# Performance work log

Hardware: AMD Instinct MI355X
Metric: run time of the kernel (lower is better)

## Reference

```python
import jax, jax.numpy as jnp
import numpy as np

M, K, N = 1024, 8192, 8192
PACK = 16  # 16 two-bit codes per int32 word


def _pack_ternary(codes):
    # codes: (N, K) int32 with values in {0,1,3} -> (N, K//16) int32
    c = codes.reshape(N, K // PACK, PACK).astype(jnp.uint32)
    shifts = (jnp.arange(PACK, dtype=jnp.uint32) * 2)
    packed = jnp.sum(c << shifts, axis=-1, dtype=jnp.uint32)
    return jax.lax.bitcast_convert_type(packed, jnp.int32)


def setup_inputs() -> dict:
    key = jax.random.key(0)
    kx, kw, kb = jax.random.split(key, 3)
    x = jax.random.normal(kx, (M, K), dtype=jnp.float16)
    # ternary codes drawn from {0,1,3} (code 2 is unused by the format)
    vals = jnp.array([0, 1, 3], dtype=jnp.int32)
    codes = vals[jax.random.randint(kw, (N, K), 0, 3)]
    packed_w = _pack_ternary(codes)
    bias = jax.random.normal(kb, (N,), dtype=jnp.float16)
    return {"x": x, "packed_w": packed_w, "bias": bias}


def _unpack(packed_w):
    # (N, K//16) int32 -> (N, K) fp16 weights with values in {0,1,3}
    shifts = jnp.arange(PACK, dtype=jnp.int32) * 2
    w = (packed_w[:, :, None] >> shifts) & 3  # mask keeps low 2 bits even with arithmetic shift
    return w.reshape(packed_w.shape[0], -1).astype(jnp.float16)


def reference(x, packed_w, bias):
    w = _unpack(packed_w)  # (N, K)
    # Y = X W^T + b, fp32 accumulation as in the CUDA/Triton GEMM, fp16 output
    y = jnp.einsum('mk,nk->mn', x, w, preferred_element_type=jnp.float32)
    y = y.astype(jnp.float16) + bias
    return y
```

## Files before the change

### kernel.cpp

```cpp
#include <hip/hip_runtime.h>
#include <hip/hip_fp16.h>
#include <stdint.h>

#define M_DIM 1024
#define N_DIM 8192
#define K_DIM 8192
#define KP    (K_DIM / 16)

#define BM 128
#define BN 128
#define BK 64
#define NTHREADS 256
#define B_STRIDE 144

#define MT_STRIDE 2097152
#define KT_STRIDE 16384

typedef _Float16 half8   __attribute__((ext_vector_type(8)));
typedef __fp16   fp16x2  __attribute__((ext_vector_type(2)));
typedef float    f32x4   __attribute__((ext_vector_type(4)));
typedef float    f32x16  __attribute__((ext_vector_type(16)));

__device__ __forceinline__ uint32_t cvt2(float a, float b) {
  fp16x2 p = __builtin_amdgcn_cvt_pkrtz(a, b);
  return __builtin_bit_cast(uint32_t, p);
}

__device__ __forceinline__ void gload_lds16(const char* g, char* l) {
  __builtin_amdgcn_global_load_lds(
      (const __attribute__((address_space(1))) void*)g,
      (__attribute__((address_space(3))) void*)l, 16, 0, 0);
}

__device__ __forceinline__ half8 dec_frag(uint32_t word, uint32_t sh) {
  const uint32_t T = 0x42063C00u;
  uint32_t h  = (word >> sh) & 0xFFFFu;
  uint32_t W  = (h & 0x3333u) | ((h << 14) & 0x33330000u);
  uint32_t c0 = __builtin_amdgcn_perm(0u, W, 0x04040200u);
  uint32_t c1 = __builtin_amdgcn_perm(0u, W, 0x04040301u);
  uint32_t s0 = (c0 * 0x1001u) & 0x03030303u;
  uint32_t s1 = (c1 * 0x1001u) & 0x03030303u;
  uint32_t P0 = __builtin_amdgcn_perm(0u, T, s0);
  uint32_t P1 = __builtin_amdgcn_perm(0u, T, s1);
  uint4 v;
  v.x = __builtin_amdgcn_perm(P0, 0u, 0x05000400u);
  v.y = __builtin_amdgcn_perm(P0, 0u, 0x07000600u);
  v.z = __builtin_amdgcn_perm(P1, 0u, 0x05000400u);
  v.w = __builtin_amdgcn_perm(P1, 0u, 0x07000600u);
  return __builtin_bit_cast(half8, v);
}

__global__ __launch_bounds__(256)
void cvt_x_t(const float* __restrict__ x, char* __restrict__ xhT) {
  __shared__ __align__(16) char st[16384];
  const int b  = blockIdx.x;
  const int mt = b >> 7, kt = b & 127;
  const int t  = threadIdx.x;
#pragma unroll
  for (int p = 0; p < 8; ++p) {
    int f   = t + 256 * p;
    int R   = f >> 4;
    int cc4 = f & 15;
    float4 v = *(const float4*)(x + (size_t)(mt * 128 + R) * K_DIM + kt * 64 + cc4 * 4);
    uint32_t w0 = cvt2(v.x, v.y), w1 = cvt2(v.z, v.w);
    int c8 = cc4 >> 1, hh = cc4 & 1;
    int i32 = R >> 5, r = R & 31, ks = c8 >> 1, q = c8 & 1;
    *(uint2*)(st + i32 * 4096 + ks * 1024 + q * 512 + r * 16 + hh * 8) = make_uint2(w0, w1);
  }
  __syncthreads();
  char* outb = xhT + (size_t)mt * MT_STRIDE + (size_t)kt * KT_STRIDE;
#pragma unroll
  for (int e = 0; e < 4; ++e) {
    int d = (e * 256 + t) * 16;
    *(uint4*)(outb + d) = *(const uint4*)(st + d);
  }
}

__global__ __launch_bounds__(NTHREADS, 2)
void ternary_gemm_dc(const char* __restrict__ xhT,
                     const int*  __restrict__ pw,
                     const float* __restrict__ bias,
                     float*       __restrict__ out) {
  __shared__ __align__(16) char Ast[3 * 16384];
  __shared__ __align__(16) char stg[3 * 2048];

  const int tid  = threadIdx.x;
  const int lane = tid & 63;
  const int w    = tid >> 6;
  const int wm   = w >> 1, wn = w & 1;
  const int bid  = blockIdx.x;
  const int mt   = bid & 7;
  const int bm   = mt * BM;
  const int bn   = (bid >> 3) * BN;

  const char* gAs = xhT + (size_t)mt * MT_STRIDE + w * 4096 + lane * 16;

  const int rT = tid >> 1, hT = tid & 1;
  const int2* gB = (const int2*)pw + (size_t)(bn + rT) * (KP / 2) + hT;
  const int stOff = rT * 16 + hT * 8;

  int rowOff[2];
#pragma unroll
  for (int j = 0; j < 2; ++j)
    rowOff[j] = (wn * 64 + j * 32 + (lane & 31)) * 16;
  const uint32_t sh = (lane >> 5) * 16;

  const char* const aPtr = Ast + wm * 8192 + lane * 16;

  f32x16 acc[2][2];
#pragma unroll
  for (int i = 0; i < 2; ++i)
#pragma unroll
    for (int j = 0; j < 2; ++j) acc[i][j] = (f32x16)(0.f);

  const int NT = K_DIM / BK;

  auto stageA = [&](int buf, int kt) {
    const char* g = gAs + (size_t)kt * KT_STRIDE;
    char* lbase = Ast + buf * 16384 + w * 4096;
#pragma unroll
    for (int e = 0; e < 4; ++e)
      gload_lds16(g + e * 1024, lbase + e * 1024);
  };

  stageA(0, 0);
  stageA(1, 1);
  int2 w0 = gB[0];
  *(int2*)(stg + stOff) = w0;
  int2 wcur = gB[2];
  __syncthreads();

  int2 wnxt;
  auto step = [&](int cur, int kt, bool counted) {
    if (kt + 2 < NT) stageA((cur + 2) % 3, kt + 2);

    uint32_t wr0[4], wr1[4];
    *(uint4*)wr0 = *(const uint4*)(stg + cur * 2048 + rowOff[0]);
    *(uint4*)wr1 = *(const uint4*)(stg + cur * 2048 + rowOff[1]);
    *(int2*)(stg + ((cur + 1) % 3) * 2048 + stOff) = wcur;
    int kn2 = (kt + 2 < NT) ? (kt + 2) : (NT - 1);
    wnxt = gB[kn2 * 2];

#pragma unroll
    for (int ks = 0; ks < 4; ++ks) {
      half8 a0 = *(const half8*)(aPtr + cur * 16384 + 0 * 4096 + ks * 1024);
      half8 a1 = *(const half8*)(aPtr + cur * 16384 + 1 * 4096 + ks * 1024);
      half8 bf0 = dec_frag(wr0[ks], sh);
      half8 bf1 = dec_frag(wr1[ks], sh);
      acc[0][0] = __builtin_amdgcn_mfma_f32_32x32x16_f16(a0, bf0, acc[0][0], 0, 0, 0);
      acc[0][1] = __builtin_amdgcn_mfma_f32_32x32x16_f16(a0, bf1, acc[0][1], 0, 0, 0);
      acc[1][0] = __builtin_amdgcn_mfma_f32_32x32x16_f16(a1, bf0, acc[1][0], 0, 0, 0);
      acc[1][1] = __builtin_amdgcn_mfma_f32_32x32x16_f16(a1, bf1, acc[1][1], 0, 0, 0);
    }

    if (counted) {
      __builtin_amdgcn_sched_barrier(0);
      asm volatile("s_waitcnt vmcnt(5) lgkmcnt(0)" ::: "memory");
      __builtin_amdgcn_s_barrier();
      asm volatile("" ::: "memory");
      __builtin_amdgcn_sched_barrier(0);
    } else {
      __syncthreads();
    }
    wcur = wnxt;
  };

  for (int kt = 0; kt < NT - 2; kt += 3) {
    step(0, kt, true);
    step(1, kt + 1, true);
    step(2, kt + 2, true);
  }
  step(0, NT - 2, false);
  step(1, NT - 1, false);

#pragma unroll
  for (int j = 0; j < 2; ++j) {
    int n = bn + wn * 64 + j * 32 + (lane & 31);
    __half hb = __float2half_rn(bias[n]);
#pragma unroll
    for (int i = 0; i < 2; ++i) {
      int mbase = bm + wm * 64 + i * 32 + 4 * (lane >> 5);
#pragma unroll
      for (int reg = 0; reg < 16; ++reg) {
        int m = mbase + (reg & 3) + 8 * (reg >> 2);
        __half hy = __float2half_rn(acc[i][j][reg]);
        out[(size_t)m * N_DIM + n] = __half2float(__hadd(hy, hb));
      }
    }
  }
}

__device__ __forceinline__ uint32_t unpack_pair16(uint32_t u, int p) {
  uint32_t c0 = (u >> (4 * p)) & 3u;
  uint32_t c1 = (u >> (4 * p + 2)) & 3u;
  uint32_t lo = (c0 & 1u) * 0x3C00u + (c0 >> 1) * 0x0600u;
  uint32_t hi = (c1 & 1u) * 0x3C00u + (c1 >> 1) * 0x0600u;
  return lo | (hi << 16);
}

__global__ __launch_bounds__(NTHREADS, 2)
void ternary_gemm(const float* __restrict__ x,
                  const int*   __restrict__ pw,
                  const float* __restrict__ bias,
                  float*       __restrict__ out) {
  __shared__ __align__(16) char AsB[128 * B_STRIDE];
  __shared__ __align__(16) char BsB[128 * B_STRIDE];

  const int tid  = threadIdx.x;
  const int lane = tid & 63;
  const int w    = tid >> 6;
  const int wm   = w >> 1, wn = w & 1;
  const int bid  = blockIdx.x;
  const int bm   = (bid & 7) * 128;
  const int bn   = (bid >> 3) * 128;

  const int rT = tid >> 1, hT = tid & 1;
  const float* gA = x + (size_t)(bm + rT) * K_DIM + hT * 32;
  char* const  lA = AsB + rT * B_STRIDE + hT * 64;
  const int2* gB = (const int2*)pw + (size_t)(bn + rT) * (KP / 2) + hT;
  char* dBp[4];
#pragma unroll
  for (int h = 0; h < 4; ++h)
    dBp[h] = BsB + rT * B_STRIDE + (hT * 4 + h) * 16;

  int offA[4][2], offB[4][2];
#pragma unroll
  for (int i = 0; i < 4; ++i)
#pragma unroll
    for (int ks = 0; ks < 2; ++ks) {
      int c = ks * 4 + (lane >> 4);
      offA[i][ks] = (wm * 64 + i * 16 + (lane & 15)) * B_STRIDE + c * 16;
      offB[i][ks] = (wn * 64 + i * 16 + (lane & 15)) * B_STRIDE + c * 16;
    }

  f32x4 acc[4][4];
#pragma unroll
  for (int i = 0; i < 4; ++i)
#pragma unroll
    for (int j = 0; j < 4; ++j)
      acc[i][j] = (f32x4){0.f, 0.f, 0.f, 0.f};

  const int NT = K_DIM / BK;
  for (int kt = 0; kt < NT; ++kt) {
    __syncthreads();
    int2 wcur = gB[kt * 2];
    float4 av[8];
#pragma unroll
    for (int v = 0; v < 8; ++v) av[v] = *(const float4*)(gA + kt * BK + v * 4);
    uint32_t d0[8], d1[8];
#pragma unroll
    for (int p = 0; p < 8; ++p) d0[p] = unpack_pair16((uint32_t)wcur.x, p);
#pragma unroll
    for (int p = 0; p < 8; ++p) d1[p] = unpack_pair16((uint32_t)wcur.y, p);
    *(uint4*)dBp[0] = make_uint4(d0[0], d0[1], d0[2], d0[3]);
    *(uint4*)dBp[1] = make_uint4(d0[4], d0[5], d0[6], d0[7]);
    *(uint4*)dBp[2] = make_uint4(d1[0], d1[1], d1[2], d1[3]);
    *(uint4*)dBp[3] = make_uint4(d1[4], d1[5], d1[6], d1[7]);
#pragma unroll
    for (int v = 0; v < 4; ++v) {
      uint4 aw;
      aw.x = cvt2(av[2 * v].x, av[2 * v].y);
      aw.y = cvt2(av[2 * v].z, av[2 * v].w);
      aw.z = cvt2(av[2 * v + 1].x, av[2 * v + 1].y);
      aw.w = cvt2(av[2 * v + 1].z, av[2 * v + 1].w);
      *(uint4*)(lA + v * 16) = aw;
    }
    __syncthreads();
#pragma unroll
    for (int ks = 0; ks < 2; ++ks) {
      half8 af[4], bf[4];
#pragma unroll
      for (int i = 0; i < 4; ++i) af[i] = *(const half8*)(AsB + offA[i][ks]);
#pragma unroll
      for (int j = 0; j < 4; ++j) bf[j] = *(const half8*)(BsB + offB[j][ks]);
#pragma unroll
      for (int i = 0; i < 4; ++i)
#pragma unroll
        for (int j = 0; j < 4; ++j)
          acc[i][j] = __builtin_amdgcn_mfma_f32_16x16x32_f16(af[i], bf[j], acc[i][j], 0, 0, 0);
    }
  }
#pragma unroll
  for (int j = 0; j < 4; ++j) {
    int n = bn + wn * 64 + j * 16 + (lane & 15);
    __half hb = __float2half_rn(bias[n]);
#pragma unroll
    for (int i = 0; i < 4; ++i) {
      int m0 = bm + wm * 64 + i * 16 + (lane >> 4) * 4;
#pragma unroll
      for (int r = 0; r < 4; ++r) {
        __half hy = __float2half_rn(acc[i][j][r]);
        out[(size_t)(m0 + r) * N_DIM + n] = __half2float(__hadd(hy, hb));
      }
    }
  }
}

extern "C" void kernel_launch(void* const* d_in, const int* in_sizes, int n_in,
                              void* d_out, int out_size, void* d_ws, size_t ws_size,
                              hipStream_t stream) {
  (void)in_sizes; (void)n_in; (void)out_size;
  const float* x    = (const float*)d_in[0];
  const int*   pwp  = (const int*)d_in[1];
  const float* bias = (const float*)d_in[2];
  float*       outp = (float*)d_out;

  const size_t need = (size_t)M_DIM * K_DIM * 2;
  if (ws_size >= need) {
    char* xhT = (char*)d_ws;
    cvt_x_t<<<8 * 128, 256, 0, stream>>>(x, xhT);
    dim3 grid((M_DIM / BM) * (N_DIM / BN));
    ternary_gemm_dc<<<grid, NTHREADS, 0, stream>>>(xhT, pwp, bias, outp);
  } else {
    dim3 grid((M_DIM / 128) * (N_DIM / 128));
    ternary_gemm<<<grid, NTHREADS, 0, stream>>>(x, pwp, bias, outp);
  }
}
```

Before: 234.5 us.

## Load packed ternary weights straight into registers, drop LDS staging

```diff
diff --git a/kernel.cpp b/kernel.cpp
--- a/kernel.cpp
+++ b/kernel.cpp
@@ -82,7 +82,6 @@
                      const float* __restrict__ bias,
                      float*       __restrict__ out) {
   __shared__ __align__(16) char Ast[3 * 16384];
-  __shared__ __align__(16) char stg[3 * 2048];
 
   const int tid  = threadIdx.x;
   const int lane = tid & 63;
@@ -95,14 +94,8 @@
 
   const char* gAs = xhT + (size_t)mt * MT_STRIDE + w * 4096 + lane * 16;
 
-  const int rT = tid >> 1, hT = tid & 1;
-  const int2* gB = (const int2*)pw + (size_t)(bn + rT) * (KP / 2) + hT;
-  const int stOff = rT * 16 + hT * 8;
-
-  int rowOff[2];
-#pragma unroll
-  for (int j = 0; j < 2; ++j)
-    rowOff[j] = (wn * 64 + j * 32 + (lane & 31)) * 16;
+  const uint4* pB0 = (const uint4*)pw + (size_t)(bn + wn * 64 + (lane & 31)) * (KP / 4);
+  const uint4* pB1 = pB0 + 32 * (KP / 4);
   const uint32_t sh = (lane >> 5) * 16;
 
   const char* const aPtr = Ast + wm * 8192 + lane * 16;
@@ -125,53 +118,64 @@
 
   stageA(0, 0);
   stageA(1, 1);
-  int2 w0 = gB[0];
-  *(int2*)(stg + stOff) = w0;
-  int2 wcur = gB[2];
+  uint4 cA0 = pB0[0], cA1 = pB1[0];
+  uint4 cB0, cB1;
   __syncthreads();
 
-  int2 wnxt;
-  auto step = [&](int cur, int kt, bool counted) {
-    if (kt + 2 < NT) stageA((cur + 2) % 3, kt + 2);
-
-    uint32_t wr0[4], wr1[4];
-    *(uint4*)wr0 = *(const uint4*)(stg + cur * 2048 + rowOff[0]);
-    *(uint4*)wr1 = *(const uint4*)(stg + cur * 2048 + rowOff[1]);
-    *(int2*)(stg + ((cur + 1) % 3) * 2048 + stOff) = wcur;
-    int kn2 = (kt + 2 < NT) ? (kt + 2) : (NT - 1);
-    wnxt = gB[kn2 * 2];
-
+  auto step = [&](int cur, int kt, uint4& c0, uint4& c1, uint4& n0, uint4& n1,
+                  bool counted) {
+    int knb = (kt + 1 < NT) ? kt + 1 : NT - 1;
+    n0 = pB0[knb];
+    n1 = pB1[knb];
+    if (kt + 2 < NT) stageA((kt + 2) % 3, kt + 2);
+
+    half8 a0[4], a1[4];
 #pragma unroll
     for (int ks = 0; ks < 4; ++ks) {
-      half8 a0 = *(const half8*)(aPtr + cur * 16384 + 0 * 4096 + ks * 1024);
-      half8 a1 = *(const half8*)(aPtr + cur * 16384 + 1 * 4096 + ks * 1024);
-      half8 bf0 = dec_frag(wr0[ks], sh);
-      half8 bf1 = dec_frag(wr1[ks], sh);
-      acc[0][0] = __builtin_amdgcn_mfma_f32_32x32x16_f16(a0, bf0, acc[0][0], 0, 0, 0);
-      acc[0][1] = __builtin_amdgcn_mfma_f32_32x32x16_f16(a0, bf1, acc[0][1], 0, 0, 0);
-      acc[1][0] = __builtin_amdgcn_mfma_f32_32x32x16_f16(a1, bf0, acc[1][0], 0, 0, 0);
-      acc[1][1] = __builtin_amdgcn_mfma_f32_32x32x16_f16(a1, bf1, acc[1][1], 0, 0, 0);
-    }
+      a0[ks] = *(const half8*)(aPtr + cur * 16384 + 0 * 4096 + ks * 1024);
+      a1[ks] = *(const half8*)(aPtr + cur * 16384 + 1 * 4096 + ks * 1024);
+    }
+
+    uint32_t wd0[4] = {c0.x, c0.y, c0.z, c0.w};
+    uint32_t wd1[4] = {c1.x, c1.y, c1.z, c1.w};
+    half8 bf0[4], bf1[4];
+#pragma unroll
+    for (int ks = 0; ks < 4; ++ks) {
+      bf0[ks] = dec_frag(wd0[ks], sh);
+      bf1[ks] = dec_frag(wd1[ks], sh);
+    }
+
+    __builtin_amdgcn_s_setprio(1);
+#pragma unroll
+    for (int ks = 0; ks < 4; ++ks) {
+      acc[0][0] = __builtin_amdgcn_mfma_f32_32x32x16_f16(a0[ks], bf0[ks], acc[0][0], 0, 0, 0);
+      acc[0][1] = __builtin_amdgcn_mfma_f32_32x32x16_f16(a0[ks], bf1[ks], acc[0][1], 0, 0, 0);
+      acc[1][0] = __builtin_amdgcn_mfma_f32_32x32x16_f16(a1[ks], bf0[ks], acc[1][0], 0, 0, 0);
+      acc[1][1] = __builtin_amdgcn_mfma_f32_32x32x16_f16(a1[ks], bf1[ks], acc[1][1], 0, 0, 0);
+    }
+    __builtin_amdgcn_s_setprio(0);
 
     if (counted) {
       __builtin_amdgcn_sched_barrier(0);
-      asm volatile("s_waitcnt vmcnt(5) lgkmcnt(0)" ::: "memory");
+      asm volatile("s_waitcnt vmcnt(6) lgkmcnt(0)" ::: "memory");
       __builtin_amdgcn_s_barrier();
       asm volatile("" ::: "memory");
       __builtin_amdgcn_sched_barrier(0);
     } else {
       __syncthreads();
     }
-    wcur = wnxt;
   };
 
-  for (int kt = 0; kt < NT - 2; kt += 3) {
-    step(0, kt, true);
-    step(1, kt + 1, true);
-    step(2, kt + 2, true);
-  }
-  step(0, NT - 2, false);
-  step(1, NT - 1, false);
+  for (int kt = 0; kt < NT - 2; kt += 6) {
+    step(0, kt,     cA0, cA1, cB0, cB1, true);
+    step(1, kt + 1, cB0, cB1, cA0, cA1, true);
+    step(2, kt + 2, cA0, cA1, cB0, cB1, true);
+    step(0, kt + 3, cB0, cB1, cA0, cA1, true);
+    step(1, kt + 4, cA0, cA1, cB0, cB1, true);
+    step(2, kt + 5, cB0, cB1, cA0, cA1, true);
+  }
+  step(0, NT - 2, cA0, cA1, cB0, cB1, false);
+  step(1, NT - 1, cB0, cB1, cA0, cA1, false);
 
 #pragma unroll
   for (int j = 0; j < 2; ++j) {
```

After: 245.2 us. 1.05x slower.

## Shrink GEMM tile to 64x128 with per-wave 64x32 outputs and higher occupancy

Applied to the files above, without the earlier changes.

```diff
diff --git a/kernel.cpp b/kernel.cpp
--- a/kernel.cpp
+++ b/kernel.cpp
@@ -7,7 +7,7 @@
 #define K_DIM 8192
 #define KP    (K_DIM / 16)
 
-#define BM 128
+#define BM 64
 #define BN 128
 #define BK 64
 #define NTHREADS 256
@@ -76,86 +76,80 @@
   }
 }
 
-__global__ __launch_bounds__(NTHREADS, 2)
+__global__ __launch_bounds__(NTHREADS, 4)
 void ternary_gemm_dc(const char* __restrict__ xhT,
                      const int*  __restrict__ pw,
                      const float* __restrict__ bias,
                      float*       __restrict__ out) {
-  __shared__ __align__(16) char Ast[3 * 16384];
+  __shared__ __align__(16) char Ast[3 * 8192];
   __shared__ __align__(16) char stg[3 * 2048];
 
   const int tid  = threadIdx.x;
   const int lane = tid & 63;
   const int w    = tid >> 6;
-  const int wm   = w >> 1, wn = w & 1;
   const int bid  = blockIdx.x;
-  const int mt   = bid & 7;
-  const int bm   = mt * BM;
-  const int bn   = (bid >> 3) * BN;
-
-  const char* gAs = xhT + (size_t)mt * MT_STRIDE + w * 4096 + lane * 16;
+  const int xcd = bid & 7;
+  const int mt  = xcd * 2 + ((bid >> 3) & 1);
+  const int nt  = bid >> 4;
+  const int bm  = mt * BM;
+  const int bn  = nt * BN;
+  const int slab = mt >> 1;
+  const int i32b = (mt & 1) * 2;
+
+  const char* gAs = xhT + (size_t)slab * MT_STRIDE + i32b * 4096 + w * 2048 + lane * 16;
 
   const int rT = tid >> 1, hT = tid & 1;
   const int2* gB = (const int2*)pw + (size_t)(bn + rT) * (KP / 2) + hT;
   const int stOff = rT * 16 + hT * 8;
 
-  int rowOff[2];
-#pragma unroll
-  for (int j = 0; j < 2; ++j)
-    rowOff[j] = (wn * 64 + j * 32 + (lane & 31)) * 16;
+  const int rowOff = (w * 32 + (lane & 31)) * 16;
   const uint32_t sh = (lane >> 5) * 16;
 
-  const char* const aPtr = Ast + wm * 8192 + lane * 16;
-
-  f32x16 acc[2][2];
-#pragma unroll
-  for (int i = 0; i < 2; ++i)
-#pragma unroll
-    for (int j = 0; j < 2; ++j) acc[i][j] = (f32x16)(0.f);
+  const char* const aPtr = Ast + lane * 16;
+
+  f32x16 acc[2];
+#pragma unroll
+  for (int i = 0; i < 2; ++i) acc[i] = (f32x16)(0.f);
 
   const int NT = K_DIM / BK;
 
   auto stageA = [&](int buf, int kt) {
     const char* g = gAs + (size_t)kt * KT_STRIDE;
-    char* lbase = Ast + buf * 16384 + w * 4096;
-#pragma unroll
-    for (int e = 0; e < 4; ++e)
+    char* lbase = Ast + buf * 8192 + w * 2048;
+#pragma unroll
+    for (int e = 0; e < 2; ++e)
       gload_lds16(g + e * 1024, lbase + e * 1024);
   };
 
   stageA(0, 0);
   stageA(1, 1);
-  int2 w0 = gB[0];
-  *(int2*)(stg + stOff) = w0;
+  int2 wfirst = gB[0];
+  *(int2*)(stg + stOff) = wfirst;
   int2 wcur = gB[2];
   __syncthreads();
 
   int2 wnxt;
   auto step = [&](int cur, int kt, bool counted) {
-    if (kt + 2 < NT) stageA((cur + 2) % 3, kt + 2);
-
-    uint32_t wr0[4], wr1[4];
-    *(uint4*)wr0 = *(const uint4*)(stg + cur * 2048 + rowOff[0]);
-    *(uint4*)wr1 = *(const uint4*)(stg + cur * 2048 + rowOff[1]);
-    *(int2*)(stg + ((cur + 1) % 3) * 2048 + stOff) = wcur;
     int kn2 = (kt + 2 < NT) ? (kt + 2) : (NT - 1);
     wnxt = gB[kn2 * 2];
+    if (kt + 2 < NT) stageA((cur + 2) % 3, kt + 2);
+
+    uint32_t wr[4];
+    *(uint4*)wr = *(const uint4*)(stg + cur * 2048 + rowOff);
+    *(int2*)(stg + ((cur + 1) % 3) * 2048 + stOff) = wcur;
 
 #pragma unroll
     for (int ks = 0; ks < 4; ++ks) {
-      half8 a0 = *(const half8*)(aPtr + cur * 16384 + 0 * 4096 + ks * 1024);
-      half8 a1 = *(const half8*)(aPtr + cur * 16384 + 1 * 4096 + ks * 1024);
-      half8 bf0 = dec_frag(wr0[ks], sh);
-      half8 bf1 = dec_frag(wr1[ks], sh);
-      acc[0][0] = __builtin_amdgcn_mfma_f32_32x32x16_f16(a0, bf0, acc[0][0], 0, 0, 0);
-      acc[0][1] = __builtin_amdgcn_mfma_f32_32x32x16_f16(a0, bf1, acc[0][1], 0, 0, 0);
-      acc[1][0] = __builtin_amdgcn_mfma_f32_32x32x16_f16(a1, bf0, acc[1][0], 0, 0, 0);
-      acc[1][1] = __builtin_amdgcn_mfma_f32_32x32x16_f16(a1, bf1, acc[1][1], 0, 0, 0);
+      half8 a0 = *(const half8*)(aPtr + cur * 8192 + 0 * 4096 + ks * 1024);
+      half8 a1 = *(const half8*)(aPtr + cur * 8192 + 1 * 4096 + ks * 1024);
+      half8 bf = dec_frag(wr[ks], sh);
+      acc[0] = __builtin_amdgcn_mfma_f32_32x32x16_f16(a0, bf, acc[0], 0, 0, 0);
+      acc[1] = __builtin_amdgcn_mfma_f32_32x32x16_f16(a1, bf, acc[1], 0, 0, 0);
     }
 
     if (counted) {
       __builtin_amdgcn_sched_barrier(0);
-      asm volatile("s_waitcnt vmcnt(5) lgkmcnt(0)" ::: "memory");
+      asm volatile("s_waitcnt vmcnt(3) lgkmcnt(0)" ::: "memory");
       __builtin_amdgcn_s_barrier();
       asm volatile("" ::: "memory");
       __builtin_amdgcn_sched_barrier(0);
@@ -173,17 +167,16 @@
   step(0, NT - 2, false);
   step(1, NT - 1, false);
 
-#pragma unroll
-  for (int j = 0; j < 2; ++j) {
-    int n = bn + wn * 64 + j * 32 + (lane & 31);
+  {
+    int n = bn + w * 32 + (lane & 31);
     __half hb = __float2half_rn(bias[n]);
 #pragma unroll
-    for (int i = 0; i < 2; ++i) {
-      int mbase = bm + wm * 64 + i * 32 + 4 * (lane >> 5);
+    for (int ig = 0; ig < 2; ++ig) {
+      int mbase = bm + ig * 32 + 4 * (lane >> 5);
 #pragma unroll
       for (int reg = 0; reg < 16; ++reg) {
         int m = mbase + (reg & 3) + 8 * (reg >> 2);
-        __half hy = __float2half_rn(acc[i][j][reg]);
+        __half hy = __float2half_rn(acc[ig][reg]);
         out[(size_t)m * N_DIM + n] = __half2float(__hadd(hy, hb));
       }
     }
```

Result: slower. 246.8 us (+5.3%).
